# Kernel tuning notes

Measured on AMD Instinct MI355X. Metric: run time of the kernel, lower is better.

## Reference

```python
import jax, jax.numpy as jnp
import numpy as np

# ---- static config (from xib add_argument defaults / chosen production sizes) ----
B, L = 16, 50            # batch, text length
LU, KU, DIM = 60, 100, 60
V, MAXVL = 2000, 10      # vocab size, max vocab word length (J)
MIN_WL, MAX_WL = 4, 10   # min/max extracted word length
NE = MAX_WL - MIN_WL + 1 # number of len_e candidates
INS_DEL_COST = 3.5       # min_ins_del_cost
UNEXTRACTED_PROB = 0.01
CONTEXT_WEIGHT = 0.1     # weight for context (conv) log-probs
NEG = -9999.9


def setup_inputs() -> dict:
    key = jax.random.key(0)
    ks = jax.random.split(key, 8)
    unit_id_seqs = jax.random.randint(ks[0], (B, L), 0, LU)
    lengths = 10 + jax.random.randint(ks[1], (B,), 0, L - 9)  # in [10, L]
    unit_repr = jax.random.normal(ks[2], (KU, DIM), jnp.float32)
    aligner_weight = 0.1 * jax.random.normal(ks[3], (LU, KU), jnp.float32)
    conv_w = jax.random.normal(ks[4], (DIM, DIM, 3), jnp.float32) / np.sqrt(3.0 * DIM)
    conv_b = jnp.zeros((DIM,), jnp.float32)
    vocab_ids = jax.random.randint(ks[5], (V, MAXVL), 0, KU)
    vocab_lengths = MIN_WL + jax.random.randint(ks[6], (V,), 0, MAXVL - MIN_WL + 1)
    return dict(unit_id_seqs=unit_id_seqs, lengths=lengths, unit_repr=unit_repr,
                aligner_weight=aligner_weight, conv_w=conv_w, conv_b=conv_b,
                vocab_ids=vocab_ids, vocab_lengths=vocab_lengths)


def reference(unit_id_seqs, lengths, unit_repr, aligner_weight, conv_w, conv_b,
              vocab_ids, vocab_lengths):
    # ---- G2P layer: embedding-as-matmul + Conv1d over length ----
    ku_char_repr = aligner_weight @ unit_repr                 # (LU, DIM)
    emb = ku_char_repr[unit_id_seqs]                          # (B, L, DIM)
    x = jnp.swapaxes(emb, 1, 2)                               # (B, DIM, L)
    y = jax.lax.conv_general_dilated(x, conv_w, (1,), 'SAME',
                                     dimension_numbers=('NCH', 'OIH', 'NCH'))
    word_repr = jnp.swapaxes(y + conv_b[None, :, None], 1, 2)  # (B, L, DIM)
    char_log_probs = jax.nn.log_softmax(ku_char_repr @ unit_repr.T, axis=-1)  # (LU, KU)
    alignment = jnp.exp(char_log_probs)
    ctx_log_probs = jax.nn.log_softmax(word_repr @ unit_repr.T, axis=-1)      # (B, L, KU)
    # per-position substitution log prob against each known unit
    pos_lp = char_log_probs[unit_id_seqs] + CONTEXT_WEIGHT * ctx_log_probs    # (B, L, KU)
    sub = pos_lp[:, :, vocab_ids]                                             # (B, L, V, J)
    sub = jnp.pad(sub, ((0, 0), (0, MAX_WL), (0, 0), (0, 0)), constant_values=NEG)
    J = MAXVL
    # ---- edit-distance style DP over (span char i, vocab char j), vectorized
    # over (batch, start position, vocab). prev[b,s,j,v] = f[i-1][j].
    j_ar = jnp.arange(J + 1, dtype=sub.dtype)
    prev = jnp.broadcast_to((-INS_DEL_COST * j_ar)[None, None, :, None], (B, L, J + 1, V))
    vl_idx = jnp.broadcast_to(vocab_lengths[None, None, None, :].astype(jnp.int32), (B, L, 1, V))
    lls = []
    for i in range(1, MAX_WL + 1):          # fixed small loop (<=10)
        sub_i = sub[:, i - 1:i - 1 + L]     # (B, L, V, J): char at position s+i-1
        row = [jnp.full((B, L, V), -INS_DEL_COST * i, dtype=sub.dtype)]
        for j in range(1, J + 1):           # fixed small loop (<=10)
            diag = prev[:, :, j - 1, :] + sub_i[:, :, :, j - 1]
            up = prev[:, :, j, :] - INS_DEL_COST
            left = row[j - 1] - INS_DEL_COST
            row.append(jnp.maximum(diag, jnp.maximum(up, left)))
        prev = jnp.stack(row, axis=2)       # (B, L, J+1, V)
        if i >= MIN_WL:                     # matched ll for word length i
            lls.append(jnp.take_along_axis(prev, vl_idx, axis=2)[:, :, 0, :])
    ll = jnp.stack(lls, axis=2)             # (B, L, NE, V) = matches.ll
    # ---- viability mask + unextracted penalty, pick best candidate ----
    starts = jnp.arange(L)
    word_lens = MIN_WL + jnp.arange(NE)
    viable = (starts[None, :, None] + word_lens[None, None, :]) <= lengths[:, None, None]  # (B,L,NE)
    unextracted = (lengths[:, None, None] - word_lens[None, None, :]).astype(ll.dtype)     # (B,1,NE)
    score = (ll + jnp.where(viable, 0.0, NEG)[..., None]
             + (unextracted * np.log(UNEXTRACTED_PROB))[..., None, :, None][:, 0])
    flat = score.reshape(B, L * NE * V)
    best_idx = jnp.argmax(flat, axis=1)
    best_matched_ll = jnp.max(flat, axis=1)
    start = best_idx // (NE * V)
    e_idx = (best_idx // V) % NE
    best_matched_vocab = best_idx % V
    end = start + MIN_WL + e_idx - 1
    return start, end, best_matched_ll, best_matched_vocab, alignment
```

## Files before the change

### kernel.cpp

```cpp
#include <hip/hip_runtime.h>
#include <math.h>
#include <stdint.h>

#define B_ 16
#define L_ 50
#define LU_ 60
#define KU_ 100
#define DIM_ 60
#define V_ 2000
#define MAXVL_ 10
#define MIN_WL_ 4
#define MAX_WL_ 10
#define NE_ 7
#define IDC_ 3.5f
#define LOG_UNEXT_ (-4.6051701859880913680359829093687f)
#define CTXW_ 0.1f
#define NQ_ 13

#define WS_PLP  0
#define WS_BEST_BYTES (80000u * 4u)
#define BEST_STRIDE 8

#define URP_ 61
#define CWP_ 61
#define TSP_ 12

__global__ __launch_bounds__(256) void ctx_kernel(
    const int* __restrict__ uid,
    const float* __restrict__ unit_repr,
    const float* __restrict__ aligner_w,
    const float* __restrict__ conv_w,
    const float* __restrict__ conv_b,
    float* __restrict__ ws_plp,
    float* __restrict__ out_align,
    unsigned long long* __restrict__ g_best)
{
  int blk = blockIdx.x;
  int b = blk / NQ_, q = blk % NQ_;
  int l0 = 4 * q;
  int npos = (l0 + 4 <= L_) ? 4 : (L_ - l0);
  int alr = (blk < LU_) ? blk : -1;
  int t = threadIdx.x;

  __shared__ float s_ur[KU_ * URP_];
  __shared__ float s_cw[3 * DIM_ * CWP_];
  __shared__ float s_aw[7 * KU_];
  __shared__ float s_kx[7 * DIM_];
  __shared__ float swr[4 * DIM_];
  __shared__ float sclp[4 * KU_];
  __shared__ float sctx[4 * KU_];
  __shared__ float salg[KU_];
  __shared__ float sls[9];

  if (blk == 0 && t < B_) g_best[t * BEST_STRIDE] = 0ull;

  const float4* ur4 = (const float4*)unit_repr;
  for (int k = t; k < (KU_ * DIM_) / 4; k += 256) {
    float4 v = ur4[k];
    int i0 = 4 * k;
    s_ur[((i0 + 0) / DIM_) * URP_ + ((i0 + 0) % DIM_)] = v.x;
    s_ur[((i0 + 1) / DIM_) * URP_ + ((i0 + 1) % DIM_)] = v.y;
    s_ur[((i0 + 2) / DIM_) * URP_ + ((i0 + 2) % DIM_)] = v.z;
    s_ur[((i0 + 3) / DIM_) * URP_ + ((i0 + 3) % DIM_)] = v.w;
  }
  const float4* cw4 = (const float4*)conv_w;
  for (int k = t; k < (DIM_ * DIM_ * 3) / 4; k += 256) {
    float4 v = cw4[k];
    int i0 = 4 * k;
    float vv[4] = {v.x, v.y, v.z, v.w};
#pragma unroll
    for (int e = 0; e < 4; ++e) {
      int idx = i0 + e;
      int o = idx / (3 * DIM_), id = idx % (3 * DIM_);
      s_cw[id * CWP_ + o] = vv[e];
    }
  }
  for (int i = t; i < 7 * KU_; i += 256) {
    int m = i / KU_, k = i - m * KU_;
    float w = 0.f;
    if (m < 6) {
      int ld = l0 - 1 + m;
      if (ld >= 0 && ld < L_) {
        int u = uid[b * L_ + ld];
        w = aligner_w[u * KU_ + k];
      }
    } else if (alr >= 0) {
      w = aligner_w[alr * KU_ + k];
    }
    s_aw[i] = w;
  }
  __syncthreads();

  for (int idx = t; idx < 7 * DIM_; idx += 256) {
    int m = idx / DIM_, c = idx - m * DIM_;
    float acc = 0.f;
    for (int k = 0; k < KU_; ++k) acc += s_aw[m * KU_ + k] * s_ur[k * URP_ + c];
    s_kx[idx] = acc;
  }
  __syncthreads();

  for (int idx = t; idx < 240 + 4 * KU_; idx += 256) {
    if (idx < 240) {
      int p = idx / DIM_, o = idx - p * DIM_;
      float acc = conv_b[o];
      for (int i = 0; i < DIM_; ++i) {
        acc += s_kx[(p + 0) * DIM_ + i] * s_cw[(i * 3 + 0) * CWP_ + o];
        acc += s_kx[(p + 1) * DIM_ + i] * s_cw[(i * 3 + 1) * CWP_ + o];
        acc += s_kx[(p + 2) * DIM_ + i] * s_cw[(i * 3 + 2) * CWP_ + o];
      }
      swr[p * DIM_ + o] = acc;
    } else {
      int r = idx - 240;
      int p = r / KU_, j = r - p * KU_;
      float acc = 0.f;
      for (int d = 0; d < DIM_; ++d) acc += s_kx[(p + 1) * DIM_ + d] * s_ur[j * URP_ + d];
      sclp[r] = acc;
    }
  }
  __syncthreads();

  for (int idx = t; idx < 4 * KU_ + KU_; idx += 256) {
    if (idx < 4 * KU_) {
      int p = idx / KU_, j = idx - p * KU_;
      float acc = 0.f;
      for (int d = 0; d < DIM_; ++d) acc += swr[p * DIM_ + d] * s_ur[j * URP_ + d];
      sctx[idx] = acc;
    } else {
      int j = idx - 4 * KU_;
      float acc = 0.f;
      for (int d = 0; d < DIM_; ++d) acc += s_kx[6 * DIM_ + d] * s_ur[j * URP_ + d];
      salg[j] = acc;
    }
  }
  __syncthreads();

  {
    int g = t >> 5, lane = t & 31;
#pragma unroll
    for (int round = 0; round < 2; ++round) {
      int r = round * 8 + g;
      if (r < 9) {
        const float* arr = (r == 8) ? salg
                          : ((r & 1) ? &sctx[(r >> 1) * KU_] : &sclp[(r >> 1) * KU_]);
        float v1 = arr[lane];
        float v2 = arr[32 + lane];
        float v3 = arr[64 + lane];
        float v4 = (lane < KU_ - 96) ? arr[96 + lane] : -1e30f;
        float mx = fmaxf(fmaxf(v1, v2), fmaxf(v3, v4));
#pragma unroll
        for (int off = 16; off > 0; off >>= 1)
          mx = fmaxf(mx, __shfl_xor(mx, off));
        float s = expf(v1 - mx) + expf(v2 - mx) + expf(v3 - mx) +
                  ((lane < KU_ - 96) ? expf(v4 - mx) : 0.f);
#pragma unroll
        for (int off = 16; off > 0; off >>= 1)
          s += __shfl_xor(s, off);
        if (lane == 0) sls[r] = mx + logf(s);
      }
    }
  }
  __syncthreads();

  for (int idx = t; idx < 4 * KU_; idx += 256) {
    int p = idx / KU_, j = idx - p * KU_;
    if (p < npos) {
      float pos = (sclp[idx] - sls[2 * p]) + CTXW_ * (sctx[idx] - sls[2 * p + 1]);
      ws_plp[(b * L_ + l0 + p) * KU_ + j] = pos;
    }
  }
  if (alr >= 0 && t < KU_)
    out_align[alr * KU_ + t] = expf(salg[t] - sls[8]);
}

__global__ __launch_bounds__(256) void dp_kernel(
    const int* __restrict__ lengths,
    const int* __restrict__ vocab_ids,
    const int* __restrict__ vocab_lengths,
    const float* __restrict__ ws_plp,
    unsigned long long* __restrict__ g_best)
{
  int bl = blockIdx.x;
  int b = bl / L_, l = bl % L_;
  int len_b = lengths[b];
  int imax = len_b - l;
  if (imax > MAX_WL_) imax = MAX_WL_;
  if (imax < MIN_WL_) return;

  __shared__ float sT[KU_ * TSP_];
  __shared__ unsigned long long swave[4];
  int t = threadIdx.x;
  {
    int n = imax * KU_;
    for (int idx = t; idx < n; idx += 256) {
      int i = idx / KU_, k = idx - i * KU_;
      sT[k * TSP_ + i] = ws_plp[(bl + i) * KU_ + k];
    }
  }
  __syncthreads();

  int v0 = blockIdx.y * 512 + t;
  int v1 = v0 + 256;
  bool has1 = (v1 < V_);
  unsigned p0[3] = {0u, 0u, 0u}, p1[3] = {0u, 0u, 0u};
#pragma unroll
  for (int j = 0; j < MAXVL_; ++j)
    p0[j >> 2] |= ((unsigned)vocab_ids[v0 * MAXVL_ + j]) << ((j & 3) * 8);
  if (has1) {
#pragma unroll
    for (int j = 0; j < MAXVL_; ++j)
      p1[j >> 2] |= ((unsigned)vocab_ids[v1 * MAXVL_ + j]) << ((j & 3) * 8);
  }
  int vlen0 = vocab_lengths[v0];
  int vlen1 = has1 ? vocab_lengths[v1] : 0;

  float A0[MAXVL_ + 1], A1[MAXVL_ + 1];
#pragma unroll
  for (int i = 0; i <= MAXVL_; ++i) {
    A0[i] = -IDC_ * (float)i;
    A1[i] = A0[i];
  }
  unsigned long long bestKey = 0ull;

#pragma unroll
  for (int j = 1; j <= MAXVL_; ++j) {
    int k0 = (int)((p0[(j - 1) >> 2] >> (((j - 1) & 3) * 8)) & 0xFFu);
    int k1 = (int)((p1[(j - 1) >> 2] >> (((j - 1) & 3) * 8)) & 0xFFu);
    const float* c0 = &sT[k0 * TSP_];
    const float* c1 = &sT[k1 * TSP_];
    float4 a0 = *(const float4*)(c0);
    float4 m0 = *(const float4*)(c0 + 4);
    float2 e0 = *(const float2*)(c0 + 8);
    float4 a1 = *(const float4*)(c1);
    float4 m1 = *(const float4*)(c1 + 4);
    float2 e1 = *(const float2*)(c1 + 8);
    float s0[MAXVL_] = {a0.x, a0.y, a0.z, a0.w, m0.x, m0.y, m0.z, m0.w, e0.x, e0.y};
    float s1[MAXVL_] = {a1.x, a1.y, a1.z, a1.w, m1.x, m1.y, m1.z, m1.w, e1.x, e1.y};
    float B0[MAXVL_ + 1], B1[MAXVL_ + 1];
    B0[0] = -IDC_ * (float)j;
    B1[0] = B0[0];
#pragma unroll
    for (int i = 1; i <= MAXVL_; ++i) {
      B0[i] = fmaxf(A0[i - 1] + s0[i - 1], fmaxf(A0[i], B0[i - 1]) - IDC_);
      B1[i] = fmaxf(A1[i - 1] + s1[i - 1], fmaxf(A1[i], B1[i - 1]) - IDC_);
    }
    if (j == vlen0) {
#pragma unroll
      for (int e = 0; e < NE_; ++e) {
        int i = MIN_WL_ + e;
        if (i <= imax) {
          float score = B0[i] + (float)(len_b - i) * LOG_UNEXT_;
          unsigned int idx = (unsigned int)(l * (NE_ * V_) + e * V_ + v0);
          unsigned int u = __float_as_uint(score);
          u = (u & 0x80000000u) ? ~u : (u | 0x80000000u);
          unsigned long long key =
              ((unsigned long long)u << 32) | (unsigned long long)(~idx);
          if (key > bestKey) bestKey = key;
        }
      }
    }
    if (j == vlen1) {
#pragma unroll
      for (int e = 0; e < NE_; ++e) {
        int i = MIN_WL_ + e;
        if (i <= imax) {
          float score = B1[i] + (float)(len_b - i) * LOG_UNEXT_;
          unsigned int idx = (unsigned int)(l * (NE_ * V_) + e * V_ + v1);
          unsigned int u = __float_as_uint(score);
          u = (u & 0x80000000u) ? ~u : (u | 0x80000000u);
          unsigned long long key =
              ((unsigned long long)u << 32) | (unsigned long long)(~idx);
          if (key > bestKey) bestKey = key;
        }
      }
    }
#pragma unroll
    for (int i = 0; i <= MAXVL_; ++i) { A0[i] = B0[i]; A1[i] = B1[i]; }
  }

#pragma unroll
  for (int off = 32; off > 0; off >>= 1) {
    unsigned long long o = __shfl_down(bestKey, off);
    if (o > bestKey) bestKey = o;
  }
  int wid = t >> 6;
  if ((t & 63) == 0) swave[wid] = bestKey;
  __syncthreads();
  if (t == 0) {
    unsigned long long k0 = swave[0];
    for (int w = 1; w < 4; ++w)
      if (swave[w] > k0) k0 = swave[w];
    atomicMax(g_best + (size_t)b * BEST_STRIDE, k0);
  }
}

__global__ void decode_kernel(const unsigned long long* __restrict__ g_best,
                              float* __restrict__ out)
{
  int t = threadIdx.x;
  if (t < B_) {
    unsigned long long key = g_best[t * BEST_STRIDE];
    unsigned int u = (unsigned int)(key >> 32);
    unsigned int idx = ~((unsigned int)(key & 0xFFFFFFFFull));
    unsigned int bits = (u & 0x80000000u) ? (u & 0x7FFFFFFFu) : ~u;
    float val = __uint_as_float(bits);
    int start = (int)(idx / (NE_ * V_));
    int rem = (int)(idx % (NE_ * V_));
    int e = rem / V_;
    int vv = rem % V_;
    out[t] = (float)start;
    out[B_ + t] = (float)(start + MIN_WL_ + e - 1);
    out[2 * B_ + t] = val;
    out[3 * B_ + t] = (float)vv;
  }
}

extern "C" void kernel_launch(void* const* d_in, const int* in_sizes, int n_in,
                              void* d_out, int out_size, void* d_ws, size_t ws_size,
                              hipStream_t stream)
{
  const int* uid            = (const int*)d_in[0];
  const int* lengths        = (const int*)d_in[1];
  const float* unit_repr    = (const float*)d_in[2];
  const float* aligner_w    = (const float*)d_in[3];
  const float* conv_w       = (const float*)d_in[4];
  const float* conv_b       = (const float*)d_in[5];
  const int* vocab_ids      = (const int*)d_in[6];
  const int* vocab_lengths  = (const int*)d_in[7];
  float* out = (float*)d_out;
  float* ws_f = (float*)d_ws;
  unsigned long long* g_best =
      (unsigned long long*)((char*)d_ws + WS_BEST_BYTES);

  ctx_kernel<<<B_ * NQ_, 256, 0, stream>>>(uid, unit_repr, aligner_w, conv_w,
                                           conv_b, ws_f + WS_PLP, out + 4 * B_,
                                           g_best);
  dim3 g3(B_ * L_, 4);
  dp_kernel<<<g3, 256, 0, stream>>>(lengths, vocab_ids, vocab_lengths,
                                    ws_f + WS_PLP, g_best);
  decode_kernel<<<1, 64, 0, stream>>>(g_best, out);
}
```

Baseline: 113.0 us.

## Sort vocab by length into packed records and skip DP rows past word length

```diff
diff --git a/kernel.cpp b/kernel.cpp
--- a/kernel.cpp
+++ b/kernel.cpp
@@ -20,6 +20,7 @@
 #define WS_PLP  0
 #define WS_BEST_BYTES (80000u * 4u)
 #define BEST_STRIDE 8
+#define WS_VPACK_BYTES (WS_BEST_BYTES + 1024u)
 
 #define URP_ 61
 #define CWP_ 61
@@ -31,16 +32,50 @@
     const float* __restrict__ aligner_w,
     const float* __restrict__ conv_w,
     const float* __restrict__ conv_b,
+    const int* __restrict__ vocab_ids,
+    const int* __restrict__ vocab_lengths,
     float* __restrict__ ws_plp,
     float* __restrict__ out_align,
-    unsigned long long* __restrict__ g_best)
+    unsigned long long* __restrict__ g_best,
+    int* __restrict__ vpack)
 {
   int blk = blockIdx.x;
+  int t = threadIdx.x;
+
+  if (blk == B_ * NQ_) {
+    __shared__ unsigned cnt[NE_];
+    if (t < NE_) cnt[t] = 0u;
+    __syncthreads();
+    for (int v = t; v < V_; v += 256)
+      atomicAdd(&cnt[vocab_lengths[v] - MIN_WL_], 1u);
+    __syncthreads();
+    if (t == 0) {
+      unsigned s = 0;
+      for (int e = 0; e < NE_; ++e) { unsigned c = cnt[e]; cnt[e] = s; s += c; }
+    }
+    __syncthreads();
+    for (int v = t; v < V_; v += 256) {
+      int vl = vocab_lengths[v];
+      unsigned dst = atomicAdd(&cnt[vl - MIN_WL_], 1u);
+      unsigned q0 = 0u, q1 = 0u, q2 = 0u;
+#pragma unroll
+      for (int j = 0; j < 4; ++j) q0 |= ((unsigned)vocab_ids[v * MAXVL_ + j]) << (j * 8);
+#pragma unroll
+      for (int j = 0; j < 4; ++j) q1 |= ((unsigned)vocab_ids[v * MAXVL_ + 4 + j]) << (j * 8);
+#pragma unroll
+      for (int j = 0; j < 2; ++j) q2 |= ((unsigned)vocab_ids[v * MAXVL_ + 8 + j]) << (j * 8);
+      int4 w;
+      w.x = (int)q0; w.y = (int)q1; w.z = (int)q2;
+      w.w = (int)((unsigned)vl | ((unsigned)v << 8));
+      ((int4*)vpack)[dst] = w;
+    }
+    return;
+  }
+
   int b = blk / NQ_, q = blk % NQ_;
   int l0 = 4 * q;
   int npos = (l0 + 4 <= L_) ? 4 : (L_ - l0);
   int alr = (blk < LU_) ? blk : -1;
-  int t = threadIdx.x;
 
   __shared__ float s_ur[KU_ * URP_];
   __shared__ float s_cw[3 * DIM_ * CWP_];
@@ -93,8 +128,16 @@
 
   for (int idx = t; idx < 7 * DIM_; idx += 256) {
     int m = idx / DIM_, c = idx - m * DIM_;
+    const float4* aw4 = (const float4*)&s_aw[m * KU_];
     float acc = 0.f;
-    for (int k = 0; k < KU_; ++k) acc += s_aw[m * KU_ + k] * s_ur[k * URP_ + c];
+    for (int k4 = 0; k4 < KU_ / 4; ++k4) {
+      float4 a = aw4[k4];
+      int k = 4 * k4;
+      acc += a.x * s_ur[(k + 0) * URP_ + c];
+      acc += a.y * s_ur[(k + 1) * URP_ + c];
+      acc += a.z * s_ur[(k + 2) * URP_ + c];
+      acc += a.w * s_ur[(k + 3) * URP_ + c];
+    }
     s_kx[idx] = acc;
   }
   __syncthreads();
@@ -102,18 +145,40 @@
   for (int idx = t; idx < 240 + 4 * KU_; idx += 256) {
     if (idx < 240) {
       int p = idx / DIM_, o = idx - p * DIM_;
+      const float4* x04 = (const float4*)&s_kx[(p + 0) * DIM_];
+      const float4* x14 = (const float4*)&s_kx[(p + 1) * DIM_];
+      const float4* x24 = (const float4*)&s_kx[(p + 2) * DIM_];
       float acc = conv_b[o];
-      for (int i = 0; i < DIM_; ++i) {
-        acc += s_kx[(p + 0) * DIM_ + i] * s_cw[(i * 3 + 0) * CWP_ + o];
-        acc += s_kx[(p + 1) * DIM_ + i] * s_cw[(i * 3 + 1) * CWP_ + o];
-        acc += s_kx[(p + 2) * DIM_ + i] * s_cw[(i * 3 + 2) * CWP_ + o];
+      for (int i4 = 0; i4 < DIM_ / 4; ++i4) {
+        float4 x0 = x04[i4], x1 = x14[i4], x2 = x24[i4];
+        int i = 4 * i4;
+        acc += x0.x * s_cw[((i + 0) * 3 + 0) * CWP_ + o];
+        acc += x1.x * s_cw[((i + 0) * 3 + 1) * CWP_ + o];
+        acc += x2.x * s_cw[((i + 0) * 3 + 2) * CWP_ + o];
+        acc += x0.y * s_cw[((i + 1) * 3 + 0) * CWP_ + o];
+        acc += x1.y * s_cw[((i + 1) * 3 + 1) * CWP_ + o];
+        acc += x2.y * s_cw[((i + 1) * 3 + 2) * CWP_ + o];
+        acc += x0.z * s_cw[((i + 2) * 3 + 0) * CWP_ + o];
+        acc += x1.z * s_cw[((i + 2) * 3 + 1) * CWP_ + o];
+        acc += x2.z * s_cw[((i + 2) * 3 + 2) * CWP_ + o];
+        acc += x0.w * s_cw[((i + 3) * 3 + 0) * CWP_ + o];
+        acc += x1.w * s_cw[((i + 3) * 3 + 1) * CWP_ + o];
+        acc += x2.w * s_cw[((i + 3) * 3 + 2) * CWP_ + o];
       }
       swr[p * DIM_ + o] = acc;
     } else {
       int r = idx - 240;
       int p = r / KU_, j = r - p * KU_;
+      const float4* kx4 = (const float4*)&s_kx[(p + 1) * DIM_];
       float acc = 0.f;
-      for (int d = 0; d < DIM_; ++d) acc += s_kx[(p + 1) * DIM_ + d] * s_ur[j * URP_ + d];
+      for (int d4 = 0; d4 < DIM_ / 4; ++d4) {
+        float4 x = kx4[d4];
+        int d = 4 * d4;
+        acc += x.x * s_ur[j * URP_ + d + 0];
+        acc += x.y * s_ur[j * URP_ + d + 1];
+        acc += x.z * s_ur[j * URP_ + d + 2];
+        acc += x.w * s_ur[j * URP_ + d + 3];
+      }
       sclp[r] = acc;
     }
   }
@@ -122,13 +187,29 @@
   for (int idx = t; idx < 4 * KU_ + KU_; idx += 256) {
     if (idx < 4 * KU_) {
       int p = idx / KU_, j = idx - p * KU_;
+      const float4* w4 = (const float4*)&swr[p * DIM_];
       float acc = 0.f;
-      for (int d = 0; d < DIM_; ++d) acc += swr[p * DIM_ + d] * s_ur[j * URP_ + d];
+      for (int d4 = 0; d4 < DIM_ / 4; ++d4) {
+        float4 x = w4[d4];
+        int d = 4 * d4;
+        acc += x.x * s_ur[j * URP_ + d + 0];
+        acc += x.y * s_ur[j * URP_ + d + 1];
+        acc += x.z * s_ur[j * URP_ + d + 2];
+        acc += x.w * s_ur[j * URP_ + d + 3];
+      }
       sctx[idx] = acc;
     } else {
       int j = idx - 4 * KU_;
+      const float4* kx4 = (const float4*)&s_kx[6 * DIM_];
       float acc = 0.f;
-      for (int d = 0; d < DIM_; ++d) acc += s_kx[6 * DIM_ + d] * s_ur[j * URP_ + d];
+      for (int d4 = 0; d4 < DIM_ / 4; ++d4) {
+        float4 x = kx4[d4];
+        int d = 4 * d4;
+        acc += x.x * s_ur[j * URP_ + d + 0];
+        acc += x.y * s_ur[j * URP_ + d + 1];
+        acc += x.z * s_ur[j * URP_ + d + 2];
+        acc += x.w * s_ur[j * URP_ + d + 3];
+      }
       salg[j] = acc;
     }
   }
@@ -174,9 +255,8 @@
 
 __global__ __launch_bounds__(256) void dp_kernel(
     const int* __restrict__ lengths,
-    const int* __restrict__ vocab_ids,
-    const int* __restrict__ vocab_lengths,
     const float* __restrict__ ws_plp,
+    const int* __restrict__ vpack,
     unsigned long long* __restrict__ g_best)
 {
   int bl = blockIdx.x;
@@ -198,20 +278,17 @@
   }
   __syncthreads();
 
-  int v0 = blockIdx.y * 512 + t;
-  int v1 = v0 + 256;
-  bool has1 = (v1 < V_);
-  unsigned p0[3] = {0u, 0u, 0u}, p1[3] = {0u, 0u, 0u};
-#pragma unroll
-  for (int j = 0; j < MAXVL_; ++j)
-    p0[j >> 2] |= ((unsigned)vocab_ids[v0 * MAXVL_ + j]) << ((j & 3) * 8);
-  if (has1) {
-#pragma unroll
-    for (int j = 0; j < MAXVL_; ++j)
-      p1[j >> 2] |= ((unsigned)vocab_ids[v1 * MAXVL_ + j]) << ((j & 3) * 8);
-  }
-  int vlen0 = vocab_lengths[v0];
-  int vlen1 = has1 ? vocab_lengths[v1] : 0;
+  int p = blockIdx.y * 256 + t;
+  const int4* vp4 = (const int4*)vpack;
+  int4 w0 = (2 * p < V_) ? vp4[2 * p] : make_int4(0, 0, 0, 0);
+  int4 w1 = (2 * p + 1 < V_) ? vp4[2 * p + 1] : make_int4(0, 0, 0, 0);
+  unsigned p0[3] = {(unsigned)w0.x, (unsigned)w0.y, (unsigned)w0.z};
+  unsigned p1[3] = {(unsigned)w1.x, (unsigned)w1.y, (unsigned)w1.z};
+  int vlen0 = (int)((unsigned)w0.w & 0xFFu);
+  int vlen1 = (int)((unsigned)w1.w & 0xFFu);
+  int v0 = (int)(((unsigned)w0.w) >> 8);
+  int v1 = (int)(((unsigned)w1.w) >> 8);
+  int jmax = (vlen0 > vlen1) ? vlen0 : vlen1;
 
   float A0[MAXVL_ + 1], A1[MAXVL_ + 1];
 #pragma unroll
@@ -223,58 +300,60 @@
 
 #pragma unroll
   for (int j = 1; j <= MAXVL_; ++j) {
-    int k0 = (int)((p0[(j - 1) >> 2] >> (((j - 1) & 3) * 8)) & 0xFFu);
-    int k1 = (int)((p1[(j - 1) >> 2] >> (((j - 1) & 3) * 8)) & 0xFFu);
-    const float* c0 = &sT[k0 * TSP_];
-    const float* c1 = &sT[k1 * TSP_];
-    float4 a0 = *(const float4*)(c0);
-    float4 m0 = *(const float4*)(c0 + 4);
-    float2 e0 = *(const float2*)(c0 + 8);
-    float4 a1 = *(const float4*)(c1);
-    float4 m1 = *(const float4*)(c1 + 4);
-    float2 e1 = *(const float2*)(c1 + 8);
-    float s0[MAXVL_] = {a0.x, a0.y, a0.z, a0.w, m0.x, m0.y, m0.z, m0.w, e0.x, e0.y};
-    float s1[MAXVL_] = {a1.x, a1.y, a1.z, a1.w, m1.x, m1.y, m1.z, m1.w, e1.x, e1.y};
-    float B0[MAXVL_ + 1], B1[MAXVL_ + 1];
-    B0[0] = -IDC_ * (float)j;
-    B1[0] = B0[0];
-#pragma unroll
-    for (int i = 1; i <= MAXVL_; ++i) {
-      B0[i] = fmaxf(A0[i - 1] + s0[i - 1], fmaxf(A0[i], B0[i - 1]) - IDC_);
-      B1[i] = fmaxf(A1[i - 1] + s1[i - 1], fmaxf(A1[i], B1[i - 1]) - IDC_);
-    }
-    if (j == vlen0) {
-#pragma unroll
-      for (int e = 0; e < NE_; ++e) {
-        int i = MIN_WL_ + e;
-        if (i <= imax) {
-          float score = B0[i] + (float)(len_b - i) * LOG_UNEXT_;
-          unsigned int idx = (unsigned int)(l * (NE_ * V_) + e * V_ + v0);
-          unsigned int u = __float_as_uint(score);
-          u = (u & 0x80000000u) ? ~u : (u | 0x80000000u);
-          unsigned long long key =
-              ((unsigned long long)u << 32) | (unsigned long long)(~idx);
-          if (key > bestKey) bestKey = key;
+    if (j <= jmax) {
+      int k0 = (int)((p0[(j - 1) >> 2] >> (((j - 1) & 3) * 8)) & 0xFFu);
+      int k1 = (int)((p1[(j - 1) >> 2] >> (((j - 1) & 3) * 8)) & 0xFFu);
+      const float* c0 = &sT[k0 * TSP_];
+      const float* c1 = &sT[k1 * TSP_];
+      float4 a0 = *(const float4*)(c0);
+      float4 m0 = *(const float4*)(c0 + 4);
+      float2 e0 = *(const float2*)(c0 + 8);
+      float4 a1 = *(const float4*)(c1);
+      float4 m1 = *(const float4*)(c1 + 4);
+      float2 e1 = *(const float2*)(c1 + 8);
+      float s0[MAXVL_] = {a0.x, a0.y, a0.z, a0.w, m0.x, m0.y, m0.z, m0.w, e0.x, e0.y};
+      float s1[MAXVL_] = {a1.x, a1.y, a1.z, a1.w, m1.x, m1.y, m1.z, m1.w, e1.x, e1.y};
+      float B0[MAXVL_ + 1], B1[MAXVL_ + 1];
+      B0[0] = -IDC_ * (float)j;
+      B1[0] = B0[0];
+#pragma unroll
+      for (int i = 1; i <= MAXVL_; ++i) {
+        B0[i] = fmaxf(A0[i - 1] + s0[i - 1], fmaxf(A0[i], B0[i - 1]) - IDC_);
+        B1[i] = fmaxf(A1[i - 1] + s1[i - 1], fmaxf(A1[i], B1[i - 1]) - IDC_);
+      }
+      if (j == vlen0) {
+#pragma unroll
+        for (int e = 0; e < NE_; ++e) {
+          int i = MIN_WL_ + e;
+          if (i <= imax) {
+            float score = B0[i] + (float)(len_b - i) * LOG_UNEXT_;
+            unsigned int idx = (unsigned int)(l * (NE_ * V_) + e * V_ + v0);
+            unsigned int u = __float_as_uint(score);
+            u = (u & 0x80000000u) ? ~u : (u | 0x80000000u);
+            unsigned long long key =
+                ((unsigned long long)u << 32) | (unsigned long long)(~idx);
+            if (key > bestKey) bestKey = key;
+          }
         }
       }
-    }
-    if (j == vlen1) {
-#pragma unroll
-      for (int e = 0; e < NE_; ++e) {
-        int i = MIN_WL_ + e;
-        if (i <= imax) {
-          float score = B1[i] + (float)(len_b - i) * LOG_UNEXT_;
-          unsigned int idx = (unsigned int)(l * (NE_ * V_) + e * V_ + v1);
-          unsigned int u = __float_as_uint(score);
-          u = (u & 0x80000000u) ? ~u : (u | 0x80000000u);
-          unsigned long long key =
-              ((unsigned long long)u << 32) | (unsigned long long)(~idx);
-          if (key > bestKey) bestKey = key;
+      if (j == vlen1) {
+#pragma unroll
+        for (int e = 0; e < NE_; ++e) {
+          int i = MIN_WL_ + e;
+          if (i <= imax) {
+            float score = B1[i] + (float)(len_b - i) * LOG_UNEXT_;
+            unsigned int idx = (unsigned int)(l * (NE_ * V_) + e * V_ + v1);
+            unsigned int u = __float_as_uint(score);
+            u = (u & 0x80000000u) ? ~u : (u | 0x80000000u);
+            unsigned long long key =
+                ((unsigned long long)u << 32) | (unsigned long long)(~idx);
+            if (key > bestKey) bestKey = key;
+          }
         }
       }
-    }
-#pragma unroll
-    for (int i = 0; i <= MAXVL_; ++i) { A0[i] = B0[i]; A1[i] = B1[i]; }
+#pragma unroll
+      for (int i = 0; i <= MAXVL_; ++i) { A0[i] = B0[i]; A1[i] = B1[i]; }
+    }
   }
 
 #pragma unroll
@@ -330,12 +409,13 @@
   float* ws_f = (float*)d_ws;
   unsigned long long* g_best =
       (unsigned long long*)((char*)d_ws + WS_BEST_BYTES);
-
-  ctx_kernel<<<B_ * NQ_, 256, 0, stream>>>(uid, unit_repr, aligner_w, conv_w,
-                                           conv_b, ws_f + WS_PLP, out + 4 * B_,
-                                           g_best);
+  int* vpack = (int*)((char*)d_ws + WS_VPACK_BYTES);
+
+  ctx_kernel<<<B_ * NQ_ + 1, 256, 0, stream>>>(uid, unit_repr, aligner_w,
+                                               conv_w, conv_b, vocab_ids,
+                                               vocab_lengths, ws_f + WS_PLP,
+                                               out + 4 * B_, g_best, vpack);
   dim3 g3(B_ * L_, 4);
-  dp_kernel<<<g3, 256, 0, stream>>>(lengths, vocab_ids, vocab_lengths,
-                                    ws_f + WS_PLP, g_best);
+  dp_kernel<<<g3, 256, 0, stream>>>(lengths, ws_f + WS_PLP, vpack, g_best);
   decode_kernel<<<1, 64, 0, stream>>>(g_best, out);
 }
```

Measured after the change: 102.3 us. 1.1x faster.
